# Kernel tuning notes

Hardware: AMD Instinct MI355X
Metric: run time of the kernel (lower is better)

The kernel has to match this reference:

```python
import jax, jax.numpy as jnp
import numpy as np

# lower-triangular (row, col) positions in the packed order used by the torch loop:
# index order is (j,i) for j in 0..2, i in 0..j -> (0,0),(1,0),(1,1),(2,0),(2,1),(2,2)
_ROWS = jnp.array([0, 1, 1, 2, 2, 2])
_COLS = jnp.array([0, 0, 1, 0, 1, 2])


def setup_inputs() -> dict:
    key = jax.random.key(0)
    bn, seq_len = 4096, 1024
    chol_cov = jax.random.normal(key, (bn, seq_len, 6), dtype=jnp.float32)
    return {"chol_cov": chol_cov}


def reference(chol_cov) -> jnp.ndarray:
    bn, seq_len, _ = chol_cov.shape
    # scatter packed values into lower-triangular 3x3 L: [bn, seq, 3, 3]
    L = jnp.zeros((bn, seq_len, 3, 3), dtype=chol_cov.dtype)
    L = L.at[..., _ROWS, _COLS].set(chol_cov)
    # Q = L @ L^T, batched tiny 3x3 matmul -> symmetric covariance
    Q = jnp.einsum('bsij,bskj->bsik', L, L)
    return Q
```

## Files before the change

kernel.cpp:

```cpp
#include <hip/hip_runtime.h>


__global__ __launch_bounds__(256) void chol_to_cov_kernel(
    const float* __restrict__ in, float* __restrict__ out, int n_items) {
  const int t = blockIdx.x * blockDim.x + threadIdx.x;
  const long long base = (long long)t * 4;
  if (base >= n_items) return;

  if (base + 4 <= n_items) {
    const float4* in4 = (const float4*)(in) + (long long)t * 6;
    float4* out4 = (float4*)(out) + (long long)t * 9;

    float s[24];
    float4 v;
#pragma unroll
    for (int k = 0; k < 6; k++) {
      v = in4[k];
      s[k * 4 + 0] = v.x;
      s[k * 4 + 1] = v.y;
      s[k * 4 + 2] = v.z;
      s[k * 4 + 3] = v.w;
    }

    float q[36];
#pragma unroll
    for (int i = 0; i < 4; i++) {
      const float a = s[i * 6 + 0];
      const float b = s[i * 6 + 1];
      const float c = s[i * 6 + 2];
      const float d = s[i * 6 + 3];
      const float e = s[i * 6 + 4];
      const float f = s[i * 6 + 5];
      const float q00 = a * a;
      const float q01 = a * b;
      const float q02 = a * d;
      const float q11 = b * b + c * c;
      const float q12 = b * d + c * e;
      const float q22 = d * d + e * e + f * f;
      q[i * 9 + 0] = q00;
      q[i * 9 + 1] = q01;
      q[i * 9 + 2] = q02;
      q[i * 9 + 3] = q01;
      q[i * 9 + 4] = q11;
      q[i * 9 + 5] = q12;
      q[i * 9 + 6] = q02;
      q[i * 9 + 7] = q12;
      q[i * 9 + 8] = q22;
    }

#pragma unroll
    for (int k = 0; k < 9; k++) {
      out4[k] = make_float4(q[k * 4 + 0], q[k * 4 + 1], q[k * 4 + 2],
                            q[k * 4 + 3]);
    }
  } else {
    for (long long it = base; it < n_items; it++) {
      const float a = in[it * 6 + 0];
      const float b = in[it * 6 + 1];
      const float c = in[it * 6 + 2];
      const float d = in[it * 6 + 3];
      const float e = in[it * 6 + 4];
      const float f = in[it * 6 + 5];
      float* o = out + it * 9;
      o[0] = a * a;
      o[1] = a * b;
      o[2] = a * d;
      o[3] = a * b;
      o[4] = b * b + c * c;
      o[5] = b * d + c * e;
      o[6] = a * d;
      o[7] = b * d + c * e;
      o[8] = d * d + e * e + f * f;
    }
  }
}

extern "C" void kernel_launch(void* const* d_in, const int* in_sizes, int n_in,
                              void* d_out, int out_size, void* d_ws,
                              size_t ws_size, hipStream_t stream) {
  const float* in = (const float*)d_in[0];
  float* out = (float*)d_out;
  const int n_items = in_sizes[0] / 6;
  const int n_threads = (n_items + 3) / 4;
  const int block = 256;
  const int grid = (n_threads + block - 1) / block;
  chol_to_cov_kernel<<<grid, block, 0, stream>>>(in, out, n_items);
}
```

Baseline: 255.7 us.

## Stage input and output through shared memory for coalesced global access

Each block now loads 1024 packed items into LDS with fully coalesced float4 loads, computes the covariance entries into an LDS output buffer, then writes them out with coalesced float4 stores. This replaces per-thread strided float4 accesses, where adjacent threads touched addresses 96 and 144 bytes apart. The cost is about 60KB of LDS per block, which limits occupancy, plus two barriers and possible LDS bank conflicts from the stride-6 and stride-9 accesses.

```diff
diff --git a/kernel.cpp b/kernel.cpp
--- a/kernel.cpp
+++ b/kernel.cpp
@@ -1,60 +1,58 @@
 #include <hip/hip_runtime.h>
 
 
-__global__ __launch_bounds__(256) void chol_to_cov_kernel(
-    const float* __restrict__ in, float* __restrict__ out, int n_items) {
-  const int t = blockIdx.x * blockDim.x + threadIdx.x;
-  const long long base = (long long)t * 4;
-  if (base >= n_items) return;
+#define THREADS 256
+#define ITEMS_PER_BLOCK 1024
 
-  if (base + 4 <= n_items) {
-    const float4* in4 = (const float4*)(in) + (long long)t * 6;
-    float4* out4 = (float4*)(out) + (long long)t * 9;
+__global__ __launch_bounds__(THREADS) void chol_to_cov_kernel(
+    const float* __restrict__ in, float* __restrict__ out, long long n_items) {
+  __shared__ float s_in[ITEMS_PER_BLOCK * 6];
+  __shared__ float s_out[ITEMS_PER_BLOCK * 9];
 
-    float s[24];
-    float4 v;
+  const int tid = threadIdx.x;
+  const long long block_base = (long long)blockIdx.x * ITEMS_PER_BLOCK;
+
+  if (block_base + ITEMS_PER_BLOCK <= n_items) {
+    const float4* __restrict__ in4 = (const float4*)(in + block_base * 6);
+    float4* s_in4 = (float4*)s_in;
 #pragma unroll
     for (int k = 0; k < 6; k++) {
-      v = in4[k];
-      s[k * 4 + 0] = v.x;
-      s[k * 4 + 1] = v.y;
-      s[k * 4 + 2] = v.z;
-      s[k * 4 + 3] = v.w;
+      s_in4[tid + k * THREADS] = in4[tid + k * THREADS];
     }
+    __syncthreads();
 
-    float q[36];
 #pragma unroll
-    for (int i = 0; i < 4; i++) {
-      const float a = s[i * 6 + 0];
-      const float b = s[i * 6 + 1];
-      const float c = s[i * 6 + 2];
-      const float d = s[i * 6 + 3];
-      const float e = s[i * 6 + 4];
-      const float f = s[i * 6 + 5];
+    for (int k = 0; k < 4; k++) {
+      const int item = tid + k * THREADS;
+      const float* s = s_in + item * 6;
+      const float a = s[0], b = s[1], c = s[2], d = s[3], e = s[4], f = s[5];
       const float q00 = a * a;
       const float q01 = a * b;
       const float q02 = a * d;
       const float q11 = b * b + c * c;
       const float q12 = b * d + c * e;
       const float q22 = d * d + e * e + f * f;
-      q[i * 9 + 0] = q00;
-      q[i * 9 + 1] = q01;
-      q[i * 9 + 2] = q02;
-      q[i * 9 + 3] = q01;
-      q[i * 9 + 4] = q11;
-      q[i * 9 + 5] = q12;
-      q[i * 9 + 6] = q02;
-      q[i * 9 + 7] = q12;
-      q[i * 9 + 8] = q22;
+      float* o = s_out + item * 9;
+      o[0] = q00;
+      o[1] = q01;
+      o[2] = q02;
+      o[3] = q01;
+      o[4] = q11;
+      o[5] = q12;
+      o[6] = q02;
+      o[7] = q12;
+      o[8] = q22;
     }
+    __syncthreads();
 
+    float4* __restrict__ out4 = (float4*)(out + block_base * 9);
+    const float4* s_out4 = (const float4*)s_out;
 #pragma unroll
     for (int k = 0; k < 9; k++) {
-      out4[k] = make_float4(q[k * 4 + 0], q[k * 4 + 1], q[k * 4 + 2],
-                            q[k * 4 + 3]);
+      out4[tid + k * THREADS] = s_out4[tid + k * THREADS];
     }
   } else {
-    for (long long it = base; it < n_items; it++) {
+    for (long long it = block_base + tid; it < n_items; it += THREADS) {
       const float a = in[it * 6 + 0];
       const float b = in[it * 6 + 1];
       const float c = in[it * 6 + 2];
@@ -80,9 +78,8 @@
                               size_t ws_size, hipStream_t stream) {
   const float* in = (const float*)d_in[0];
   float* out = (float*)d_out;
-  const int n_items = in_sizes[0] / 6;
-  const int n_threads = (n_items + 3) / 4;
-  const int block = 256;
-  const int grid = (n_threads + block - 1) / block;
-  chol_to_cov_kernel<<<grid, block, 0, stream>>>(in, out, n_items);
+  const long long n_items = (long long)in_sizes[0] / 6;
+  const long long grid =
+      (n_items + ITEMS_PER_BLOCK - 1) / ITEMS_PER_BLOCK;
+  chol_to_cov_kernel<<<(int)grid, THREADS, 0, stream>>>(in, out, n_items);
 }
```

Result: faster. 223.6 us (-12.5%).
